# Optimization experiments

Hardware: AMD Instinct MI355X
Metric: run time of the kernel (lower is better)

The kernel has to match this reference:

```python
import jax, jax.numpy as jnp
import numpy as np


def setup_inputs() -> dict:
    key = jax.random.key(0)
    k1, k2, k3 = jax.random.split(key, 3)
    N, D = 65536, 1024
    def unit_rows(k):
        x = jax.random.normal(k, (N, D), dtype=jnp.float32)
        return x / jnp.linalg.norm(x, axis=-1, keepdims=True)
    return {
        "input_embs": unit_rows(k1),
        "neg_input_embs": unit_rows(k2),
        "image_embs": unit_rows(k3),
        "alpha": 1,
    }


def reference(input_embs, neg_input_embs, image_embs, alpha):
    # diagonal of (N,D)@(D,N) == paired row-wise dot products: O(N*D) not O(N^2*D)
    rewards_pos = jnp.sum(input_embs * image_embs, axis=-1)      # [N]
    rewards_neg = jnp.sum(neg_input_embs * image_embs, axis=-1)  # [N]
    loss = -jnp.mean(jax.nn.log_sigmoid((rewards_pos - rewards_neg) * alpha))
    return loss
```

## Files before the change

kernel.cpp:

```cpp
#include <hip/hip_runtime.h>
#include <hip/hip_bf16.h>


#define DIMS 1024
#define BLOCKS 2048
#define THREADS 256
#define WAVES_PER_BLOCK (THREADS / 64)
#define ROWS_PER_WAVE 8

__global__ __launch_bounds__(THREADS) void rewardclip_main(
    const float* __restrict__ a,
    const float* __restrict__ b,
    const float* __restrict__ c,
    const int* __restrict__ alpha_p,
    int rows,
    float* __restrict__ partials) {
  const int tid  = threadIdx.x;
  const int lane = tid & 63;
  const int wave = tid >> 6;
  const int gwave = blockIdx.x * WAVES_PER_BLOCK + wave;

  const float alpha = (float)(*alpha_p);

  float acc = 0.0f;

  const int row0 = gwave * ROWS_PER_WAVE;
#pragma unroll 1
  for (int r = 0; r < ROWS_PER_WAVE; ++r) {
    const int row = row0 + r;
    if (row >= rows) break;
    const float4* __restrict__ pa = (const float4*)(a + (size_t)row * DIMS) + lane;
    const float4* __restrict__ pb = (const float4*)(b + (size_t)row * DIMS) + lane;
    const float4* __restrict__ pc = (const float4*)(c + (size_t)row * DIMS) + lane;

    const float4 a0 = pa[0], a1 = pa[64], a2 = pa[128], a3 = pa[192];
    const float4 b0 = pb[0], b1 = pb[64], b2 = pb[128], b3 = pb[192];
    const float4 c0 = pc[0], c1 = pc[64], c2 = pc[128], c3 = pc[192];

    float d0 = 0.f, d1 = 0.f, d2 = 0.f, d3 = 0.f;
    d0 += (a0.x - b0.x) * c0.x; d0 += (a0.y - b0.y) * c0.y;
    d0 += (a0.z - b0.z) * c0.z; d0 += (a0.w - b0.w) * c0.w;
    d1 += (a1.x - b1.x) * c1.x; d1 += (a1.y - b1.y) * c1.y;
    d1 += (a1.z - b1.z) * c1.z; d1 += (a1.w - b1.w) * c1.w;
    d2 += (a2.x - b2.x) * c2.x; d2 += (a2.y - b2.y) * c2.y;
    d2 += (a2.z - b2.z) * c2.z; d2 += (a2.w - b2.w) * c2.w;
    d3 += (a3.x - b3.x) * c3.x; d3 += (a3.y - b3.y) * c3.y;
    d3 += (a3.z - b3.z) * c3.z; d3 += (a3.w - b3.w) * c3.w;

    float d = (d0 + d1) + (d2 + d3);

#pragma unroll
    for (int off = 32; off > 0; off >>= 1) d += __shfl_down(d, off, 64);

    if (lane == 0) {
      const float x = d * alpha;
      const float ls = fminf(x, 0.0f) - log1pf(__expf(-fabsf(x)));
      acc += ls;
    }
  }

  __shared__ float s[WAVES_PER_BLOCK];
  if (lane == 0) s[wave] = acc;
  __syncthreads();
  if (tid == 0) {
    float t = 0.0f;
#pragma unroll
    for (int w = 0; w < WAVES_PER_BLOCK; ++w) t += s[w];
    partials[blockIdx.x] = t;
  }
}

__global__ __launch_bounds__(THREADS) void rewardclip_finalize(
    const float* __restrict__ partials, int nparts, int rows,
    float* __restrict__ out) {
  const int tid  = threadIdx.x;
  const int lane = tid & 63;
  const int wave = tid >> 6;

  float s = 0.0f;
  for (int i = tid; i < nparts; i += THREADS) s += partials[i];

#pragma unroll
  for (int off = 32; off > 0; off >>= 1) s += __shfl_down(s, off, 64);

  __shared__ float ws[WAVES_PER_BLOCK];
  if (lane == 0) ws[wave] = s;
  __syncthreads();
  if (tid == 0) {
    float t = 0.0f;
#pragma unroll
    for (int w = 0; w < WAVES_PER_BLOCK; ++w) t += ws[w];
    out[0] = -t / (float)rows;
  }
}

extern "C" void kernel_launch(void* const* d_in, const int* in_sizes, int n_in,
                              void* d_out, int out_size, void* d_ws, size_t ws_size,
                              hipStream_t stream) {
  const float* a = (const float*)d_in[0];
  const float* b = (const float*)d_in[1];
  const float* c = (const float*)d_in[2];
  const int* alpha_p = (const int*)d_in[3];

  const int rows = in_sizes[0] / DIMS;
  float* partials = (float*)d_ws;
  float* out = (float*)d_out;

  rewardclip_main<<<BLOCKS, THREADS, 0, stream>>>(a, b, c, alpha_p, rows, partials);
  rewardclip_finalize<<<1, THREADS, 0, stream>>>(partials, BLOCKS, rows, out);
}
```

Measured before the change: 142.0 us.

## Replace finalize kernel with atomic accumulation and use grid-stride row loop

The separate finalize kernel is removed. Each block now atomically adds its scaled partial sum into the output, which is zeroed by a memset beforehand. The row mapping also changes from contiguous chunks per wave to a grid-stride loop over rows. The aim is to save one kernel launch and its dependency gap, at the cost of a memset launch, 2048 contended float atomics, and a summation order that is no longer deterministic.

```diff
diff --git a/kernel.cpp b/kernel.cpp
--- a/kernel.cpp
+++ b/kernel.cpp
@@ -6,7 +6,6 @@
 #define BLOCKS 2048
 #define THREADS 256
 #define WAVES_PER_BLOCK (THREADS / 64)
-#define ROWS_PER_WAVE 8
 
 __global__ __launch_bounds__(THREADS) void rewardclip_main(
     const float* __restrict__ a,
@@ -14,21 +13,18 @@
     const float* __restrict__ c,
     const int* __restrict__ alpha_p,
     int rows,
-    float* __restrict__ partials) {
+    float* __restrict__ out) {
   const int tid  = threadIdx.x;
   const int lane = tid & 63;
   const int wave = tid >> 6;
-  const int gwave = blockIdx.x * WAVES_PER_BLOCK + wave;
+  const int gwave  = blockIdx.x * WAVES_PER_BLOCK + wave;
+  const int nwaves = gridDim.x * WAVES_PER_BLOCK;
 
   const float alpha = (float)(*alpha_p);
 
   float acc = 0.0f;
 
-  const int row0 = gwave * ROWS_PER_WAVE;
-#pragma unroll 1
-  for (int r = 0; r < ROWS_PER_WAVE; ++r) {
-    const int row = row0 + r;
-    if (row >= rows) break;
+  for (int row = gwave; row < rows; row += nwaves) {
     const float4* __restrict__ pa = (const float4*)(a + (size_t)row * DIMS) + lane;
     const float4* __restrict__ pb = (const float4*)(b + (size_t)row * DIMS) + lane;
     const float4* __restrict__ pc = (const float4*)(c + (size_t)row * DIMS) + lane;
@@ -66,31 +62,7 @@
     float t = 0.0f;
 #pragma unroll
     for (int w = 0; w < WAVES_PER_BLOCK; ++w) t += s[w];
-    partials[blockIdx.x] = t;
-  }
-}
-
-__global__ __launch_bounds__(THREADS) void rewardclip_finalize(
-    const float* __restrict__ partials, int nparts, int rows,
-    float* __restrict__ out) {
-  const int tid  = threadIdx.x;
-  const int lane = tid & 63;
-  const int wave = tid >> 6;
-
-  float s = 0.0f;
-  for (int i = tid; i < nparts; i += THREADS) s += partials[i];
-
-#pragma unroll
-  for (int off = 32; off > 0; off >>= 1) s += __shfl_down(s, off, 64);
-
-  __shared__ float ws[WAVES_PER_BLOCK];
-  if (lane == 0) ws[wave] = s;
-  __syncthreads();
-  if (tid == 0) {
-    float t = 0.0f;
-#pragma unroll
-    for (int w = 0; w < WAVES_PER_BLOCK; ++w) t += ws[w];
-    out[0] = -t / (float)rows;
+    atomicAdd(out, t * (-1.0f / (float)rows));
   }
 }
 
@@ -103,9 +75,8 @@
   const int* alpha_p = (const int*)d_in[3];
 
   const int rows = in_sizes[0] / DIMS;
-  float* partials = (float*)d_ws;
   float* out = (float*)d_out;
 
-  rewardclip_main<<<BLOCKS, THREADS, 0, stream>>>(a, b, c, alpha_p, rows, partials);
-  rewardclip_finalize<<<1, THREADS, 0, stream>>>(partials, BLOCKS, rows, out);
+  hipMemsetAsync(out, 0, sizeof(float), stream);
+  rewardclip_main<<<BLOCKS, THREADS, 0, stream>>>(a, b, c, alpha_p, rows, out);
 }
```

After: 149.1 us. 1.05x slower.
